# Kernel tuning notes

Measured on AMD Instinct MI355X. Metric: run time of the kernel, lower is better.

## Reference

```python
import jax, jax.numpy as jnp
import numpy as np

B, D, E, H = 8192, 512, 16, 128  # batch, input_dim, num_experts, hidden_dim
EPS = 1e-5  # BatchNorm eps (torch default)


def setup_inputs() -> dict:
    key = jax.random.key(0)
    ks = iter(jax.random.split(key, 32))
    def n(shape, s=0.05):
        return jax.random.normal(next(ks), shape, dtype=jnp.float32) * s
    inp = {"x": jax.random.normal(next(ks), (B, D), dtype=jnp.float32)}
    # Router params, stacked over the 2 branches (gender, race)
    inp["rbn_gamma"] = jnp.ones((2, D), jnp.float32)
    inp["rbn_beta"] = jnp.zeros((2, D), jnp.float32)
    inp["rbn_mean"] = n((2, D))
    inp["rbn_var"] = jnp.ones((2, D), jnp.float32)
    inp["rW1"], inp["rb1"] = n((2, D, 64)), jnp.full((2, 64), 0.1, jnp.float32)
    inp["rW2"], inp["rb2"] = n((2, 64, 32)), jnp.full((2, 32), 0.1, jnp.float32)
    inp["rW3"], inp["rb3"] = n((2, 32, E)), jnp.full((2, E), 0.1, jnp.float32)
    # Expert params, stacked over [branch=2, expert=16]
    inp["ebn_gamma"] = jnp.ones((2, E, D), jnp.float32)
    inp["ebn_beta"] = jnp.zeros((2, E, D), jnp.float32)
    inp["ebn_mean"] = n((2, E, D))
    inp["ebn_var"] = jnp.ones((2, E, D), jnp.float32)
    inp["eW1"], inp["eb1"] = n((2, E, D, H)), jnp.full((2, E, H), 0.1, jnp.float32)
    inp["eW2"], inp["eb2"] = n((2, E, H, H // 2)), jnp.full((2, E, H // 2), 0.1, jnp.float32)
    inp["eW3"], inp["eb3"] = n((2, E, H // 2)), jnp.full((2, E), 0.1, jnp.float32)
    inp["branch_weights"] = jnp.array([0.5, 0.5], jnp.float32)
    return inp


def reference(x, rbn_gamma, rbn_beta, rbn_mean, rbn_var, rW1, rb1, rW2, rb2,
              rW3, rb3, ebn_gamma, ebn_beta, ebn_mean, ebn_var, eW1, eb1,
              eW2, eb2, eW3, eb3, branch_weights):
    def branch(c):
        # Router: BN(eval) -> Linear(64) -> ReLU -> Linear(32) -> ReLU -> Linear(E) -> Softmax
        xn = (x - rbn_mean[c]) * jax.lax.rsqrt(rbn_var[c] + EPS) * rbn_gamma[c] + rbn_beta[c]
        h = jax.nn.relu(xn @ rW1[c] + rb1[c])
        h = jax.nn.relu(h @ rW2[c] + rb2[c])
        rw = jax.nn.softmax(h @ rW3[c] + rb3[c], axis=1)  # [B, E]
        # Experts batched over E: per-expert BN(eval) -> Linear -> ReLU -> Linear -> ReLU -> Linear -> sigmoid
        m, v = ebn_mean[c][:, None, :], ebn_var[c][:, None, :]
        g, b = ebn_gamma[c][:, None, :], ebn_beta[c][:, None, :]
        xe = (x[None] - m) * jax.lax.rsqrt(v + EPS) * g + b          # [E, B, D]
        h1 = jax.nn.relu(jnp.einsum('ebd,edh->ebh', xe, eW1[c]) + eb1[c][:, None, :])
        h2 = jax.nn.relu(jnp.einsum('ebh,ehk->ebk', h1, eW2[c]) + eb2[c][:, None, :])
        out = jax.nn.sigmoid(jnp.einsum('ebk,ek->eb', h2, eW3[c]) + eb3[c][:, None])  # [E, B]
        return jnp.einsum('be,eb->b', rw, out)                        # weighted sum over experts
    gender_pred = branch(0)
    race_pred = branch(1)
    return branch_weights[0] * gender_pred + branch_weights[1] * race_pred
```

## Files before the change

### kernel.cpp

```cpp
#include <hip/hip_runtime.h>

typedef __attribute__((ext_vector_type(8))) short short8;
typedef __attribute__((ext_vector_type(8))) unsigned short ushort8;
typedef __attribute__((ext_vector_type(4))) unsigned short us4;
typedef __attribute__((ext_vector_type(4))) float f32x4;
typedef unsigned int u32;
typedef unsigned short u16;

#define AS_GLOBAL(p) ((const __attribute__((address_space(1))) u32*)(p))
#define AS_LDS(p) ((__attribute__((address_space(3))) u32*)(p))

#define NB 8192
#define ND 512
#define NH 128

#define OFF_XPK    0u
#define OFF_W1PK   8388608u
#define OFF_W2PK   12582912u
#define OFF_RW1PT  13107200u
#define OFF_PBIAS  13238784u
#define OFF_B1P    13369856u
#define OFF_RWT    13402112u
#define OFF_RPB    14450688u

__device__ __forceinline__ u16 f2bf(float f) {
  union { float f; u32 u; } v; v.f = f;
  return (u16)((v.u + 0x7FFFu + ((v.u >> 16) & 1u)) >> 16);
}

__global__ __launch_bounds__(256) void k_prep_all(
    const float* __restrict__ x, u16* __restrict__ xpk,
    const float* __restrict__ eg, const float* __restrict__ ebb,
    const float* __restrict__ em, const float* __restrict__ ev,
    const float* __restrict__ eW1, u16* __restrict__ w1pk, float* __restrict__ pbias,
    const float* __restrict__ eW2, u16* __restrict__ w2pk,
    const float* __restrict__ rbn_g, const float* __restrict__ rbn_b,
    const float* __restrict__ rbn_m, const float* __restrict__ rbn_v,
    const float* __restrict__ rW1,
    u16* __restrict__ rw1pt, float* __restrict__ rpb,
    float* __restrict__ out)
{
  __shared__ __align__(16) unsigned char sh[18432];
  const int blk = blockIdx.x, t = threadIdx.x;
  if (blk < 512) {
    u16* tile = (u16*)sh;
    const float* src = x + (size_t)blk * 16 * ND;
#pragma unroll
    for (int j = 0; j < 8; ++j) {
      int g = (j * 256 + t) * 4;
      float4 v = *(const float4*)(src + g);
      int row = g >> 9, col = g & 511;
      u32 byteoff = (u32)row * 1024 + (((u32)col * 2) ^ ((u32)(row & 7) << 4));
      us4 r4;
      r4[0] = f2bf(v.x); r4[1] = f2bf(v.y); r4[2] = f2bf(v.z); r4[3] = f2bf(v.w);
      *(us4*)((unsigned char*)tile + byteoff) = r4;
    }
    __syncthreads();
    const int lane = t & 63, wv = t >> 6;
    const int lr = lane & 15, q = lane >> 4;
#pragma unroll
    for (int jk = 0; jk < 4; ++jk) {
      int kb = wv * 4 + jk;
      u32 byteoff = (u32)lr * 1024 + (((u32)(kb * 64 + q * 16)) ^ ((u32)(lr & 7) << 4));
      ushort8 r = *(const ushort8*)((unsigned char*)tile + byteoff);
      *(ushort8*)(xpk + ((u32)(blk * 16 + kb) * 64 + lane) * 8) = r;
    }
  } else if (blk < 768) {
    float* sa = (float*)sh;
    float* sc = sa + 64;
    u16* tile = (u16*)(sh + 512);
    float* pb2 = (float*)(sh + 512 + 16896);
    const int pair = (blk - 512) >> 3, dc = (blk - 512) & 7;
    const int d0 = dc * 64;
    if (t < 64) {
      int d = pair * ND + d0 + t;
      float a = eg[d] * rsqrtf(ev[d] + 1e-5f);
      sa[t] = a;
      sc[t] = ebb[d] - em[d] * a;
    }
    __syncthreads();
    const int h = t & 127, pr = t >> 7;
    float acc = 0.f;
    const float* src = eW1 + (size_t)pair * ND * NH + (size_t)d0 * NH;
#pragma unroll
    for (int i = 0; i < 32; ++i) {
      int dl = i * 2 + pr;
      float w = src[dl * NH + h];
      tile[dl * 132 + h] = f2bf(w * sa[dl]);
      acc += w * sc[dl];
    }
    pb2[pr * 128 + h] = acc;
    __syncthreads();
    {
      const int lane = t & 63, wv = t >> 6;
      const int lr = lane & 15, q = lane >> 4;
#pragma unroll
      for (int ff = 0; ff < 4; ++ff) {
        int f = wv * 4 + ff;
        int kbl = f >> 3, nb = f & 7;
        ushort8 r;
#pragma unroll
        for (int j = 0; j < 8; ++j)
          r[j] = tile[(kbl * 32 + q * 8 + j) * 132 + nb * 16 + lr];
        *(ushort8*)(w1pk + ((u32)((pair * 16 + dc * 2 + kbl) * 8 + nb)) * 512
                    + (u32)lane * 8) = r;
      }
    }
    if (t < 128) pbias[(u32)(pair * 8 + dc) * 128 + t] = pb2[t] + pb2[128 + t];
  } else if (blk < 800) {
    const int pair = blk - 768;
    const float* w2 = eW2 + (size_t)pair * NH * 64;
    int n = t & 63, kk = t >> 6;
    for (int k = kk * 32; k < kk * 32 + 32; ++k) {
      u32 dst = ((u32)((pair * 4 + (k >> 5)) * 4 + (n >> 4))) * 512
              + (((k >> 3) & 3) * 16 + (n & 15)) * 8 + (k & 7);
      w2pk[dst] = f2bf(w2[k * 64 + n]);
    }
  } else if (blk < 832) {
    float* red = (float*)sh;
    const int b = blk - 800, c = b >> 4, dc = b & 15;
    const int n = t & 63, dg = t >> 6;
    const int d0 = dc * 32 + dg * 8;
    const float* g  = rbn_g + c * ND;
    const float* bb = rbn_b + c * ND;
    const float* m  = rbn_m + c * ND;
    const float* vv = rbn_v + c * ND;
    const float* w1 = rW1 + (size_t)c * ND * 64;
    float acc = 0.f;
    ushort8 r;
#pragma unroll
    for (int j = 0; j < 8; ++j) {
      int d = d0 + j;
      float a  = g[d] * rsqrtf(vv[d] + 1e-5f);
      float cc = bb[d] - m[d] * a;
      float w  = w1[d * 64 + n];
      r[j] = f2bf(a * w);
      acc += cc * w;
    }
    *(ushort8*)(rw1pt + ((u32)(c * 64 + n)) * 512 + d0) = r;
    red[dg * 64 + n] = acc;
    __syncthreads();
    if (t < 64)
      rpb[(u32)(c * 16 + dc) * 64 + t] = red[t] + red[64 + t] + red[128 + t] + red[192 + t];
  } else {
    float4 z; z.x = 0.f; z.y = 0.f; z.z = 0.f; z.w = 0.f;
    float4* o4 = (float4*)out;
#pragma unroll
    for (int j = 0; j < 8; ++j) o4[t * 8 + j] = z;
  }
}

__global__ __launch_bounds__(256) void k_router(
    const u16* __restrict__ xpk, const u16* __restrict__ rw1pt,
    const float* __restrict__ rb1, const float* __restrict__ rpb,
    const float* __restrict__ rW2,
    const float* __restrict__ rb2, const float* __restrict__ rW3,
    const float* __restrict__ rb3, float* __restrict__ rwT,
    const float* __restrict__ pbias, const float* __restrict__ eb1,
    float* __restrict__ b1p)
{
  __shared__ float h1l[64][65];
  __shared__ float h2l[64][33];
  __shared__ float w2s[2048];
  __shared__ float w3s[512];
  __shared__ float rb1s[64];
  const int tid = threadIdx.x;
  if (blockIdx.x >= 256) {
    const int pair = blockIdx.x - 256;
    if (tid < 128) {
      float s = eb1[pair * NH + tid];
#pragma unroll
      for (int dc = 0; dc < 8; ++dc) s += pbias[(u32)(pair * 8 + dc) * 128 + tid];
      b1p[pair * NH + tid] = s;
    }
    return;
  }
  const int lane = tid & 63;
  const int wv = tid >> 6;
  const int q = lane >> 4;
  const int lr = lane & 15;
  const int c = blockIdx.x >> 7;
  const int r0 = (blockIdx.x & 127) * 64;
  {
    const float* W2 = rW2 + c * 2048;
    *(float4*)(w2s + tid * 8)     = *(const float4*)(W2 + tid * 8);
    *(float4*)(w2s + tid * 8 + 4) = *(const float4*)(W2 + tid * 8 + 4);
    if (tid < 128)
      *(float4*)(w3s + tid * 4) = *(const float4*)(rW3 + c * 512 + tid * 4);
    if (tid < 64) {
      float s = rb1[c * 64 + tid];
#pragma unroll
      for (int k = 0; k < 16; ++k) s += rpb[(u32)(c * 16 + k) * 64 + tid];
      rb1s[tid] = s;
    }
  }
  __syncthreads();
  f32x4 acc[4] = {};
  const u16* xfr   = xpk + ((u32)((r0 >> 4) + wv) * 16) * 512 + (u32)lane * 8;
  const u16* wbase = rw1pt + ((u32)c * 64 << 9);
  for (int kb = 0; kb < 16; ++kb) {
    short8 a = *(const short8*)(xfr + kb * 512);
#pragma unroll
    for (int u = 0; u < 4; ++u) {
      short8 b = *(const short8*)(wbase + (((u32)(u * 16 + lr)) << 9) + kb * 32 + q * 8);
      acc[u] = __builtin_amdgcn_mfma_f32_16x16x32_bf16(a, b, acc[u], 0, 0, 0);
    }
  }
#pragma unroll
  for (int u = 0; u < 4; ++u) {
    int n = u * 16 + lr;
    float bias = rb1s[n];
#pragma unroll
    for (int i = 0; i < 4; ++i) {
      float v = acc[u][i] + bias;
      h1l[wv * 16 + q * 4 + i][n] = v > 0.f ? v : 0.f;
    }
  }
  __syncthreads();
  {
    int row = tid >> 2, part = (tid & 3) * 8;
    float hv[8];
#pragma unroll
    for (int j = 0; j < 8; ++j) hv[j] = rb2[c * 32 + part + j];
#pragma unroll
    for (int k = 0; k < 64; ++k) {
      float hk = h1l[row][k];
#pragma unroll
      for (int j = 0; j < 8; ++j) hv[j] += hk * w2s[k * 32 + part + j];
    }
#pragma unroll
    for (int j = 0; j < 8; ++j) h2l[row][part + j] = hv[j] > 0.f ? hv[j] : 0.f;
  }
  __syncthreads();
  {
    int row = tid >> 2, e0 = (tid & 3) * 4;
    float lg[4];
#pragma unroll
    for (int e = 0; e < 4; ++e) {
      float a3 = rb3[c * 16 + e0 + e];
#pragma unroll
      for (int k = 0; k < 32; ++k) a3 += h2l[row][k] * w3s[k * 16 + e0 + e];
      lg[e] = a3;
    }
    float mx = fmaxf(fmaxf(lg[0], lg[1]), fmaxf(lg[2], lg[3]));
    mx = fmaxf(mx, __shfl_xor(mx, 1, 64));
    mx = fmaxf(mx, __shfl_xor(mx, 2, 64));
    float sm = 0.f;
#pragma unroll
    for (int e = 0; e < 4; ++e) { lg[e] = __expf(lg[e] - mx); sm += lg[e]; }
    sm += __shfl_xor(sm, 1, 64);
    sm += __shfl_xor(sm, 2, 64);
    float inv = 1.f / sm;
#pragma unroll
    for (int e = 0; e < 4; ++e)
      rwT[(u32)(c * 16 + e0 + e) * NB + r0 + row] = lg[e] * inv;
  }
}

__global__ __launch_bounds__(256, 2) void k_expert(
    const u16* __restrict__ xpk, const float* __restrict__ b1p,
    const u16* __restrict__ w2pk,
    const float* __restrict__ eb2, const float* __restrict__ eW3,
    const float* __restrict__ eb3, const float* __restrict__ rwT,
    const float* __restrict__ bw, float* __restrict__ out)
{
  extern __shared__ __align__(16) unsigned char smem[];
  const int tid = threadIdx.x;
  const int lane = tid & 63;
  const int wv = tid >> 6;
  const int q = lane >> 4, lr = lane & 15;
  const int wr = wv >> 1;
  const int p  = wv & 1;
  const int xcd  = blockIdx.x & 7;
  const int slot = blockIdx.x >> 3;
  const int pt   = xcd * 2 + (slot & 1);
  const int bt   = slot >> 1;
  const int pr0  = pt * 2;
  const int r0   = bt * 128;
  const u32 lane16 = (u32)lane * 16;

  u32 soff[6], sstep[6], slds[6];
#pragma unroll
  for (int j = 0; j < 6; ++j) {
    int f = wv * 6 + j;
    if (f < 8) {
      soff[j]  = ((u32)(bt * 8 + f) * 16) * 512 + (u32)lane * 8;
      sstep[j] = 512;
      slds[j]  = (u32)f * 1024;
    } else {
      int g = f - 8;
      soff[j]  = 4194304u + ((u32)(pr0 + (g >> 3)) * 128 + (g & 7)) * 512 + (u32)lane * 8;
      sstep[j] = 4096;
      slds[j]  = 8192 + (u32)g * 1024;
    }
  }

#define STAGE(BUF, KB) do { \
  _Pragma("unroll") for (int j_ = 0; j_ < 6; ++j_) \
    __builtin_amdgcn_global_load_lds( \
        AS_GLOBAL(xpk + soff[j_] + (u32)(KB) * sstep[j_]), \
        AS_LDS(smem + (BUF) + slds[j_]), 16, 0, 0); \
  } while (0)

  f32x4 acc[4][8] = {};

  STAGE(0u, 0);
  STAGE(24576u, 1);
  asm volatile("s_waitcnt vmcnt(6)" ::: "memory");
  __builtin_amdgcn_s_barrier();

#pragma unroll
  for (int kb = 0; kb < 16; ++kb) {
    const u32 BUF = (u32)(kb % 3) * 24576u;
    if (kb < 14) {
      STAGE((u32)((kb + 2) % 3) * 24576u, kb + 2);
      __builtin_amdgcn_sched_barrier(0);
    }
    short8 a_[4], b_[8];
#pragma unroll
    for (int t = 0; t < 4; ++t)
      a_[t] = *(const short8*)(smem + BUF + (u32)(wr * 4 + t) * 1024 + lane16);
#pragma unroll
    for (int u = 0; u < 8; ++u)
      b_[u] = *(const short8*)(smem + BUF + 8192 + (u32)(p * 8 + u) * 1024 + lane16);
#pragma unroll
    for (int t = 0; t < 4; ++t)
#pragma unroll
      for (int u = 0; u < 8; ++u)
        acc[t][u] = __builtin_amdgcn_mfma_f32_16x16x32_bf16(a_[t], b_[u], acc[t][u], 0, 0, 0);
    if (kb < 14)       asm volatile("s_waitcnt vmcnt(6)" ::: "memory");
    else if (kb == 14) asm volatile("s_waitcnt vmcnt(0)" ::: "memory");
    if (kb < 15) __builtin_amdgcn_s_barrier();
  }
#undef STAGE

  __syncthreads();

  {
    float b1w[8];
#pragma unroll
    for (int u = 0; u < 8; ++u) b1w[u] = b1p[(pr0 + p) * NH + u * 16 + lr];
#pragma unroll
    for (int t = 0; t < 4; ++t)
#pragma unroll
      for (int u = 0; u < 8; ++u) {
        const int rb = wr * 4 + t;
        const int kb2 = u >> 1;
        const int q2 = (u & 1) * 2 + (lr >> 3), j2 = lr & 7;
#pragma unroll
        for (int i = 0; i < 4; ++i) {
          float v = acc[t][u][i] + b1w[u];
          v = v > 0.f ? v : 0.f;
          u32 byteoff = ((u32)(((p * 8 + rb) * 4 + kb2) * 64 + q2 * 16 + q * 4 + i)) * 16 + j2 * 2;
          *(u16*)(smem + byteoff) = f2bf(v);
        }
      }
  }
  __syncthreads();

  f32x4 acc2[2][2][4] = {};
#pragma unroll
  for (int pl = 0; pl < 2; ++pl)
#pragma unroll
    for (int kk = 0; kk < 4; ++kk) {
      short8 a2[2], b2v[4];
#pragma unroll
      for (int t2 = 0; t2 < 2; ++t2)
        a2[t2] = *(const short8*)(smem + (u32)(((pl * 8 + wv * 2 + t2) * 4 + kk)) * 1024 + lane16);
#pragma unroll
      for (int u2 = 0; u2 < 4; ++u2)
        b2v[u2] = *(const short8*)(w2pk + ((u32)(((pr0 + pl) * 4 + kk) * 4 + u2)) * 512 + (u32)lane * 8);
#pragma unroll
      for (int t2 = 0; t2 < 2; ++t2)
#pragma unroll
        for (int u2 = 0; u2 < 4; ++u2)
          acc2[pl][t2][u2] = __builtin_amdgcn_mfma_f32_16x16x32_bf16(a2[t2], b2v[u2], acc2[pl][t2][u2], 0, 0, 0);
    }

#pragma unroll
  for (int pl = 0; pl < 2; ++pl) {
    const int pairG = pr0 + pl;
    float bb2[4], bw3v[4];
#pragma unroll
    for (int u2 = 0; u2 < 4; ++u2) {
      bb2[u2]  = eb2[pairG * 64 + u2 * 16 + lr];
      bw3v[u2] = eW3[pairG * 64 + u2 * 16 + lr];
    }
    float b3 = eb3[pairG];
    float bwc = bw[pairG >> 4];
#pragma unroll
    for (int t2 = 0; t2 < 2; ++t2) {
      float pp[4] = {0.f, 0.f, 0.f, 0.f};
#pragma unroll
      for (int u2 = 0; u2 < 4; ++u2)
#pragma unroll
        for (int i = 0; i < 4; ++i) {
          float h = acc2[pl][t2][u2][i] + bb2[u2];
          h = h > 0.f ? h : 0.f;
          pp[i] += h * bw3v[u2];
        }
#pragma unroll
      for (int m = 1; m < 16; m <<= 1)
#pragma unroll
        for (int i = 0; i < 4; ++i) pp[i] += __shfl_xor(pp[i], m, 64);
      if (lr == 0) {
#pragma unroll
        for (int i = 0; i < 4; ++i) {
          int row = wv * 32 + t2 * 16 + q * 4 + i;
          float z = pp[i] + b3;
          float s = 1.f / (1.f + __expf(-z));
          float rw = rwT[(u32)pairG * NB + r0 + row];
          atomicAdd(out + r0 + row, bwc * rw * s);
        }
      }
    }
  }
}

extern "C" void kernel_launch(void* const* d_in, const int* in_sizes, int n_in,
                              void* d_out, int out_size, void* d_ws, size_t ws_size,
                              hipStream_t stream) {
  const float* x     = (const float*)d_in[0];
  const float* rbn_g = (const float*)d_in[1];
  const float* rbn_b = (const float*)d_in[2];
  const float* rbn_m = (const float*)d_in[3];
  const float* rbn_v = (const float*)d_in[4];
  const float* rW1   = (const float*)d_in[5];
  const float* rb1   = (const float*)d_in[6];
  const float* rW2   = (const float*)d_in[7];
  const float* rb2   = (const float*)d_in[8];
  const float* rW3   = (const float*)d_in[9];
  const float* rb3   = (const float*)d_in[10];
  const float* ebn_g = (const float*)d_in[11];
  const float* ebn_b = (const float*)d_in[12];
  const float* ebn_m = (const float*)d_in[13];
  const float* ebn_v = (const float*)d_in[14];
  const float* eW1   = (const float*)d_in[15];
  const float* eb1   = (const float*)d_in[16];
  const float* eW2   = (const float*)d_in[17];
  const float* eb2   = (const float*)d_in[18];
  const float* eW3   = (const float*)d_in[19];
  const float* eb3   = (const float*)d_in[20];
  const float* bw    = (const float*)d_in[21];

  char* ws = (char*)d_ws;
  u16*   xpk   = (u16*)(ws + OFF_XPK);
  u16*   w1pk  = (u16*)(ws + OFF_W1PK);
  u16*   w2pk  = (u16*)(ws + OFF_W2PK);
  u16*   rw1pt = (u16*)(ws + OFF_RW1PT);
  float* pbias = (float*)(ws + OFF_PBIAS);
  float* b1p   = (float*)(ws + OFF_B1P);
  float* rwT   = (float*)(ws + OFF_RWT);
  float* rpb   = (float*)(ws + OFF_RPB);
  float* outf  = (float*)d_out;

  k_prep_all<<<dim3(833), dim3(256), 0, stream>>>(
      x, xpk, ebn_g, ebn_b, ebn_m, ebn_v, eW1, w1pk, pbias, eW2, w2pk,
      rbn_g, rbn_b, rbn_m, rbn_v, rW1, rw1pt, rpb, outf);
  k_router<<<dim3(288), dim3(256), 0, stream>>>(
      xpk, rw1pt, rb1, rpb, rW2, rb2, rW3, rb3, rwT, pbias, eb1, b1p);
  k_expert<<<dim3(1024), dim3(256), 73728, stream>>>(
      xpk, b1p, w2pk, eb2, eW3, eb3, rwT, bw, outf);
}
```

Measured before the change: 73.97 us.

## Enlarge expert GEMM tile to 256 rows with 8 waves and ping-pong scheduling

The expert kernel now uses 512-thread blocks, each covering 256 batch rows instead of 128. The main loop splits each k-step into two MFMA phases with barriers and s_setprio, so LDS reads and MFMA work from different waves can interleave. The second-layer GEMM and epilogue now run in two halves over the row tile. The aim is better reuse of the staged weight tile and better MFMA issue. In exchange it runs half as many blocks at one block per CU, uses more LDS, and adds extra barriers.

After: 79.39 us. 1.07x slower.

```diff
diff --git a/kernel.cpp b/kernel.cpp
--- a/kernel.cpp
+++ b/kernel.cpp
@@ -257,7 +257,7 @@
   }
 }
 
-__global__ __launch_bounds__(256, 2) void k_expert(
+__global__ __launch_bounds__(512, 1) void k_expert(
     const u16* __restrict__ xpk, const float* __restrict__ b1p,
     const u16* __restrict__ w2pk,
     const float* __restrict__ eb2, const float* __restrict__ eW3,
@@ -269,152 +269,175 @@
   const int lane = tid & 63;
   const int wv = tid >> 6;
   const int q = lane >> 4, lr = lane & 15;
-  const int wr = wv >> 1;
-  const int p  = wv & 1;
+  const int wr = wv >> 2;
+  const int wc = wv & 3;
+  const int pl = wc >> 1;
+  const int ph = wc & 1;
   const int xcd  = blockIdx.x & 7;
   const int slot = blockIdx.x >> 3;
   const int pt   = xcd * 2 + (slot & 1);
   const int bt   = slot >> 1;
   const int pr0  = pt * 2;
-  const int r0   = bt * 128;
+  const int r0   = bt * 256;
   const u32 lane16 = (u32)lane * 16;
 
-  u32 soff[6], sstep[6], slds[6];
-#pragma unroll
-  for (int j = 0; j < 6; ++j) {
-    int f = wv * 6 + j;
-    if (f < 8) {
-      soff[j]  = ((u32)(bt * 8 + f) * 16) * 512 + (u32)lane * 8;
+  u32 soff[4], sstep[4], slds[4];
+#pragma unroll
+  for (int j = 0; j < 4; ++j) {
+    int f = wv * 4 + j;
+    if (f < 16) {
+      soff[j]  = ((u32)(bt * 16 + f) * 16) * 512 + (u32)lane * 8;
       sstep[j] = 512;
       slds[j]  = (u32)f * 1024;
     } else {
-      int g = f - 8;
+      int g = f - 16;
       soff[j]  = 4194304u + ((u32)(pr0 + (g >> 3)) * 128 + (g & 7)) * 512 + (u32)lane * 8;
       sstep[j] = 4096;
-      slds[j]  = 8192 + (u32)g * 1024;
+      slds[j]  = 16384 + (u32)g * 1024;
     }
   }
 
 #define STAGE(BUF, KB) do { \
-  _Pragma("unroll") for (int j_ = 0; j_ < 6; ++j_) \
+  _Pragma("unroll") for (int j_ = 0; j_ < 4; ++j_) \
     __builtin_amdgcn_global_load_lds( \
         AS_GLOBAL(xpk + soff[j_] + (u32)(KB) * sstep[j_]), \
         AS_LDS(smem + (BUF) + slds[j_]), 16, 0, 0); \
   } while (0)
-
-  f32x4 acc[4][8] = {};
+#define SB __builtin_amdgcn_sched_barrier(0)
+#define BAR __builtin_amdgcn_s_barrier()
+#define LGKM0 asm volatile("s_waitcnt lgkmcnt(0)" ::: "memory")
+#define RDA(T) (*(const short8*)(smem + BUF + (u32)(wr * 8 + (T)) * 1024 + lane16))
+#define RDB(U) (*(const short8*)(smem + BUF + 16384 + (u32)(wc * 4 + (U)) * 1024 + lane16))
+
+  f32x4 acc[8][4] = {};
+  short8 a_[4], b_[4];
 
   STAGE(0u, 0);
-  STAGE(24576u, 1);
-  asm volatile("s_waitcnt vmcnt(6)" ::: "memory");
-  __builtin_amdgcn_s_barrier();
+  STAGE(32768u, 1);
+  asm volatile("s_waitcnt vmcnt(4)" ::: "memory");
+  BAR;
 
 #pragma unroll
   for (int kb = 0; kb < 16; ++kb) {
-    const u32 BUF = (u32)(kb % 3) * 24576u;
-    if (kb < 14) {
-      STAGE((u32)((kb + 2) % 3) * 24576u, kb + 2);
-      __builtin_amdgcn_sched_barrier(0);
-    }
-    short8 a_[4], b_[8];
+    const u32 BUF = (u32)(kb % 3) * 32768u;
+    a_[0] = RDA(0); a_[1] = RDA(1); a_[2] = RDA(2); a_[3] = RDA(3);
+    b_[0] = RDB(0); b_[1] = RDB(1); b_[2] = RDB(2); b_[3] = RDB(3);
+    if (kb < 14) STAGE((u32)((kb + 2) % 3) * 32768u, kb + 2);
+    SB; BAR; LGKM0; SB;
+    __builtin_amdgcn_s_setprio(1);
 #pragma unroll
     for (int t = 0; t < 4; ++t)
-      a_[t] = *(const short8*)(smem + BUF + (u32)(wr * 4 + t) * 1024 + lane16);
-#pragma unroll
-    for (int u = 0; u < 8; ++u)
-      b_[u] = *(const short8*)(smem + BUF + 8192 + (u32)(p * 8 + u) * 1024 + lane16);
+#pragma unroll
+      for (int u = 0; u < 4; ++u)
+        acc[t][u] = __builtin_amdgcn_mfma_f32_16x16x32_bf16(a_[t], b_[u], acc[t][u], 0, 0, 0);
+    __builtin_amdgcn_s_setprio(0);
+    SB; BAR;
+    a_[0] = RDA(4); a_[1] = RDA(5); a_[2] = RDA(6); a_[3] = RDA(7);
+    SB; BAR; LGKM0; SB;
+    __builtin_amdgcn_s_setprio(1);
 #pragma unroll
     for (int t = 0; t < 4; ++t)
 #pragma unroll
-      for (int u = 0; u < 8; ++u)
-        acc[t][u] = __builtin_amdgcn_mfma_f32_16x16x32_bf16(a_[t], b_[u], acc[t][u], 0, 0, 0);
-    if (kb < 14)       asm volatile("s_waitcnt vmcnt(6)" ::: "memory");
+      for (int u = 0; u < 4; ++u)
+        acc[4 + t][u] = __builtin_amdgcn_mfma_f32_16x16x32_bf16(a_[t], b_[u], acc[4 + t][u], 0, 0, 0);
+    __builtin_amdgcn_s_setprio(0);
+    SB;
+    if (kb < 14)       asm volatile("s_waitcnt vmcnt(4)" ::: "memory");
     else if (kb == 14) asm volatile("s_waitcnt vmcnt(0)" ::: "memory");
-    if (kb < 15) __builtin_amdgcn_s_barrier();
+    if (kb < 15) BAR;
   }
 #undef STAGE
+#undef RDA
+#undef RDB
+#undef LGKM0
+#undef BAR
 
   __syncthreads();
 
-  {
-    float b1w[8];
-#pragma unroll
-    for (int u = 0; u < 8; ++u) b1w[u] = b1p[(pr0 + p) * NH + u * 16 + lr];
-#pragma unroll
-    for (int t = 0; t < 4; ++t)
-#pragma unroll
-      for (int u = 0; u < 8; ++u) {
-        const int rb = wr * 4 + t;
-        const int kb2 = u >> 1;
-        const int q2 = (u & 1) * 2 + (lr >> 3), j2 = lr & 7;
-#pragma unroll
-        for (int i = 0; i < 4; ++i) {
-          float v = acc[t][u][i] + b1w[u];
-          v = v > 0.f ? v : 0.f;
-          u32 byteoff = ((u32)(((p * 8 + rb) * 4 + kb2) * 64 + q2 * 16 + q * 4 + i)) * 16 + j2 * 2;
-          *(u16*)(smem + byteoff) = f2bf(v);
+  float b1w[4];
+#pragma unroll
+  for (int u = 0; u < 4; ++u)
+    b1w[u] = b1p[(pr0 + pl) * NH + ph * 64 + u * 16 + lr];
+  const int pw = wv >> 2;
+  const int rq = wv & 3;
+
+#pragma unroll
+  for (int rh = 0; rh < 2; ++rh) {
+    if (wr == rh) {
+#pragma unroll
+      for (int t = 0; t < 8; ++t)
+#pragma unroll
+        for (int u = 0; u < 4; ++u) {
+          const int kb2 = ph * 2 + (u >> 1);
+          const int q2 = (u & 1) * 2 + (lr >> 3), j2 = lr & 7;
+#pragma unroll
+          for (int i = 0; i < 4; ++i) {
+            float v = acc[t][u][i] + b1w[u];
+            v = v > 0.f ? v : 0.f;
+            u32 byteoff = ((u32)(((pl * 8 + t) * 4 + kb2) * 64 + q2 * 16 + q * 4 + i)) * 16 + j2 * 2;
+            *(u16*)(smem + byteoff) = f2bf(v);
+          }
+        }
+    }
+    __syncthreads();
+
+    f32x4 acc2[2][4] = {};
+#pragma unroll
+    for (int kk = 0; kk < 4; ++kk) {
+      short8 a2[2], b2v[4];
+#pragma unroll
+      for (int t2 = 0; t2 < 2; ++t2)
+        a2[t2] = *(const short8*)(smem + (u32)(((pw * 8 + rq * 2 + t2) * 4 + kk)) * 1024 + lane16);
+#pragma unroll
+      for (int u2 = 0; u2 < 4; ++u2)
+        b2v[u2] = *(const short8*)(w2pk + ((u32)(((pr0 + pw) * 4 + kk) * 4 + u2)) * 512 + (u32)lane * 8);
+#pragma unroll
+      for (int t2 = 0; t2 < 2; ++t2)
+#pragma unroll
+        for (int u2 = 0; u2 < 4; ++u2)
+          acc2[t2][u2] = __builtin_amdgcn_mfma_f32_16x16x32_bf16(a2[t2], b2v[u2], acc2[t2][u2], 0, 0, 0);
+    }
+
+    {
+      const int pairG = pr0 + pw;
+      float bb2[4], bw3v[4];
+#pragma unroll
+      for (int u2 = 0; u2 < 4; ++u2) {
+        bb2[u2]  = eb2[pairG * 64 + u2 * 16 + lr];
+        bw3v[u2] = eW3[pairG * 64 + u2 * 16 + lr];
+      }
+      float b3 = eb3[pairG];
+      float bwc = bw[pairG >> 4];
+#pragma unroll
+      for (int t2 = 0; t2 < 2; ++t2) {
+        float pp[4] = {0.f, 0.f, 0.f, 0.f};
+#pragma unroll
+        for (int u2 = 0; u2 < 4; ++u2)
+#pragma unroll
+          for (int i = 0; i < 4; ++i) {
+            float h = acc2[t2][u2][i] + bb2[u2];
+            h = h > 0.f ? h : 0.f;
+            pp[i] += h * bw3v[u2];
+          }
+#pragma unroll
+        for (int m = 1; m < 16; m <<= 1)
+#pragma unroll
+          for (int i = 0; i < 4; ++i) pp[i] += __shfl_xor(pp[i], m, 64);
+        if (lr == 0) {
+#pragma unroll
+          for (int i = 0; i < 4; ++i) {
+            int row = r0 + rh * 128 + rq * 32 + t2 * 16 + q * 4 + i;
+            float z = pp[i] + b3;
+            float s = 1.f / (1.f + __expf(-z));
+            float rw = rwT[(u32)pairG * NB + row];
+            atomicAdd(out + row, bwc * rw * s);
+          }
         }
       }
-  }
-  __syncthreads();
-
-  f32x4 acc2[2][2][4] = {};
-#pragma unroll
-  for (int pl = 0; pl < 2; ++pl)
-#pragma unroll
-    for (int kk = 0; kk < 4; ++kk) {
-      short8 a2[2], b2v[4];
-#pragma unroll
-      for (int t2 = 0; t2 < 2; ++t2)
-        a2[t2] = *(const short8*)(smem + (u32)(((pl * 8 + wv * 2 + t2) * 4 + kk)) * 1024 + lane16);
-#pragma unroll
-      for (int u2 = 0; u2 < 4; ++u2)
-        b2v[u2] = *(const short8*)(w2pk + ((u32)(((pr0 + pl) * 4 + kk) * 4 + u2)) * 512 + (u32)lane * 8);
-#pragma unroll
-      for (int t2 = 0; t2 < 2; ++t2)
-#pragma unroll
-        for (int u2 = 0; u2 < 4; ++u2)
-          acc2[pl][t2][u2] = __builtin_amdgcn_mfma_f32_16x16x32_bf16(a2[t2], b2v[u2], acc2[pl][t2][u2], 0, 0, 0);
-    }
-
-#pragma unroll
-  for (int pl = 0; pl < 2; ++pl) {
-    const int pairG = pr0 + pl;
-    float bb2[4], bw3v[4];
-#pragma unroll
-    for (int u2 = 0; u2 < 4; ++u2) {
-      bb2[u2]  = eb2[pairG * 64 + u2 * 16 + lr];
-      bw3v[u2] = eW3[pairG * 64 + u2 * 16 + lr];
-    }
-    float b3 = eb3[pairG];
-    float bwc = bw[pairG >> 4];
-#pragma unroll
-    for (int t2 = 0; t2 < 2; ++t2) {
-      float pp[4] = {0.f, 0.f, 0.f, 0.f};
-#pragma unroll
-      for (int u2 = 0; u2 < 4; ++u2)
-#pragma unroll
-        for (int i = 0; i < 4; ++i) {
-          float h = acc2[pl][t2][u2][i] + bb2[u2];
-          h = h > 0.f ? h : 0.f;
-          pp[i] += h * bw3v[u2];
-        }
-#pragma unroll
-      for (int m = 1; m < 16; m <<= 1)
-#pragma unroll
-        for (int i = 0; i < 4; ++i) pp[i] += __shfl_xor(pp[i], m, 64);
-      if (lr == 0) {
-#pragma unroll
-        for (int i = 0; i < 4; ++i) {
-          int row = wv * 32 + t2 * 16 + q * 4 + i;
-          float z = pp[i] + b3;
-          float s = 1.f / (1.f + __expf(-z));
-          float rw = rwT[(u32)pairG * NB + r0 + row];
-          atomicAdd(out + r0 + row, bwc * rw * s);
-        }
-      }
-    }
-  }
+    }
+    __syncthreads();
+  }
+#undef SB
 }
 
 extern "C" void kernel_launch(void* const* d_in, const int* in_sizes, int n_in,
@@ -459,6 +482,6 @@
       rbn_g, rbn_b, rbn_m, rbn_v, rW1, rw1pt, rpb, outf);
   k_router<<<dim3(288), dim3(256), 0, stream>>>(
       xpk, rw1pt, rb1, rpb, rW2, rb2, rW3, rb3, rwT, pbias, eb1, b1p);
-  k_expert<<<dim3(1024), dim3(256), 73728, stream>>>(
+  k_expert<<<dim3(512), dim3(512), 98304, stream>>>(
       xpk, b1p, w2pk, eb2, eW3, eb3, rwT, bw, outf);
 }
```
